# Performance work log

Measured on AMD Instinct MI355X. Metric: run time of the kernel, lower is better.

Reference implementation:

```python
import jax, jax.numpy as jnp
import numpy as np

NEG_INF = -1e30


def setup_inputs() -> dict:
    key = jax.random.key(0)
    ks = jax.random.split(key, 7)
    N, C, B = 262144, 256, 8
    feats = jax.random.normal(ks[0], (N, C), dtype=jnp.float32)
    scores = jax.random.normal(ks[1], (N, 1), dtype=jnp.float32)
    w_reg = jax.random.normal(ks[2], (C, 6), dtype=jnp.float32) * 0.01
    w_cls = jax.random.normal(ks[3], (C, 18), dtype=jnp.float32) * 0.01
    b_cls = jax.random.normal(ks[4], (18,), dtype=jnp.float32) * 0.01
    scale = jnp.ones((1,), dtype=jnp.float32)
    batch_ids = jnp.sort(jax.random.randint(ks[5], (N,), 0, B, dtype=jnp.int32))
    return {"feats": feats, "scores": scores, "w_reg": w_reg, "w_cls": w_cls,
            "b_cls": b_cls, "scale": scale, "batch_ids": batch_ids,
            "n_batches": B, "pts_threshold": 8192}


def _prune_mask(scores, batch_ids, n_batches, k):
    # scores: [N,1]; per-batch top-k selection mask (torch.topk + scatter in original).
    s = jax.lax.stop_gradient(scores[:, 0])  # computed under no_grad in torch
    # [B, N]: score where point belongs to batch b, else -inf
    per_batch = jnp.where(batch_ids[None, :] == jnp.arange(n_batches, dtype=batch_ids.dtype)[:, None],
                          s[None, :], NEG_INF)
    kth = jax.lax.top_k(per_batch, k)[0][:, -1]  # [B] k-th largest per cloud
    return s >= kth[batch_ids]  # [N] bool


def reference(feats, scores, w_reg, w_cls, b_cls, scale, batch_ids, n_batches, pts_threshold):
    mask = _prune_mask(scores, batch_ids, n_batches, pts_threshold)
    x = feats * mask[:, None].astype(feats.dtype)  # MinkowskiPruning (fixed-shape: zero out)
    # FCAF3D heads: 1x1 sparse convs == per-point matmuls; reg goes through Scale + exp.
    bbox_pred = jnp.exp(scale[0] * (x @ w_reg))          # [N, 6]
    cls_score = x @ w_cls + b_cls                         # [N, 18]
    return jnp.concatenate([bbox_pred, cls_score], axis=-1)  # [N, 24]
```

## Files before the change

kernel.cpp:

```cpp
#include <hip/hip_runtime.h>

typedef unsigned int u32;
typedef unsigned long long u64;

#define NBINS 65536
#define MAXB 8

__device__ __forceinline__ u32 mono(float f) {
    u32 u = __float_as_uint(f);
    return (u & 0x80000000u) ? ~u : (u | 0x80000000u);
}

__global__ void k_histA(const float* __restrict__ scores, const int* __restrict__ bids,
                        u32* __restrict__ hist, int N) {
    int i = blockIdx.x * blockDim.x + threadIdx.x;
    if (i >= N) return;
    atomicAdd(&hist[(u32)bids[i] * NBINS + (mono(scores[i]) >> 16)], 1u);
}

__global__ void k_histB(const float* __restrict__ scores, const int* __restrict__ bids,
                        const u32* __restrict__ Hstar, u32* __restrict__ hist, int N) {
    int i = blockIdx.x * blockDim.x + threadIdx.x;
    if (i >= N) return;
    int b = bids[i];
    u32 key = mono(scores[i]);
    if ((key >> 16) == Hstar[b])
        atomicAdd(&hist[(u32)b * NBINS + (key & 0xFFFFu)], 1u);
}

__device__ int suffix_select(const u32* __restrict__ h, u32 target, u32& remaining_out) {
    __shared__ u32 s[256];
    __shared__ int cc_s;
    __shared__ u32 run_s;
    __shared__ int res_s;
    __shared__ u32 rem_s;
    const int t = threadIdx.x;
    if (t == 0) cc_s = -1;
    u32 tot = 0;
    const uint4* hv = (const uint4*)(h + t * 256);
#pragma unroll 8
    for (int q = 0; q < 64; ++q) { uint4 v = hv[q]; tot += v.x + v.y + v.z + v.w; }
    s[t] = tot;
    __syncthreads();
    for (int off = 1; off < 256; off <<= 1) {
        u32 add = (t + off < 256) ? s[t + off] : 0u;
        __syncthreads();
        s[t] += add;
        __syncthreads();
    }
    u32 nxt = (t == 255) ? 0u : s[t + 1];
    if (s[t] >= target && nxt < target) { cc_s = t; run_s = nxt; }
    __syncthreads();
    int cc = cc_s;
    if (cc < 0) { remaining_out = 0; return -1; }
    u32 running = run_s;
    u32 v = h[cc * 256 + t];
    __syncthreads();
    s[t] = v;
    __syncthreads();
    for (int off = 1; off < 256; off <<= 1) {
        u32 add = (t + off < 256) ? s[t + off] : 0u;
        __syncthreads();
        s[t] += add;
        __syncthreads();
    }
    u32 nxt2 = (t == 255) ? 0u : s[t + 1];
    if (running + s[t] >= target && running + nxt2 < target) {
        res_s = cc * 256 + t;
        rem_s = target - (running + nxt2);
    }
    __syncthreads();
    remaining_out = rem_s;
    return res_s;
}

__global__ void k_scanA(const u32* __restrict__ hist, const int* __restrict__ kptr,
                        u32* __restrict__ Hstar, u32* __restrict__ rB,
                        u32* __restrict__ thresh) {
    int b = blockIdx.x;
    u32 rem;
    int bin = suffix_select(hist + (size_t)b * NBINS, (u32)kptr[0], rem);
    if (threadIdx.x == 0) {
        if (bin < 0) { Hstar[b] = 0xFFFFFFFFu; rB[b] = 0u; thresh[b] = 0u; }
        else { Hstar[b] = (u32)bin; rB[b] = rem; }
    }
}

__global__ void k_scanB(const u32* __restrict__ hist, const u32* __restrict__ Hstar,
                        const u32* __restrict__ rB, u32* __restrict__ thresh) {
    int b = blockIdx.x;
    u32 H = Hstar[b];
    if (H == 0xFFFFFFFFu) return;
    u32 rem;
    int bin = suffix_select(hist + (size_t)b * NBINS, rB[b], rem);
    if (threadIdx.x == 0) thresh[b] = (H << 16) | (u32)bin;
}

__global__ __launch_bounds__(256) void k_fused(
    const float* __restrict__ feats, const float* __restrict__ scores,
    const int* __restrict__ bids, const u32* __restrict__ thresh,
    const float* __restrict__ wreg, const float* __restrict__ wcls,
    const float* __restrict__ bcls, const float* __restrict__ scalep,
    float* __restrict__ out, int N) {

    __shared__ float W[256 * 24];
    __shared__ u32 alive_idx[512];
    __shared__ u32 nAlive;
    __shared__ float defrow[24];

    float scl = scalep[0];
    for (int idx = threadIdx.x; idx < 256 * 24; idx += 256) {
        int c = idx / 24, j = idx - c * 24;
        W[idx] = (j < 6) ? scl * wreg[c * 6 + j] : wcls[c * 18 + (j - 6)];
    }
    if (threadIdx.x == 0) nAlive = 0;
    if (threadIdx.x < 24) defrow[threadIdx.x] = (threadIdx.x < 6) ? 1.0f : bcls[threadIdx.x - 6];
    __syncthreads();

    const int base = blockIdx.x * 512;
#pragma unroll
    for (int q = 0; q < 2; ++q) {
        int i = base + threadIdx.x + q * 256;
        if (i < N) {
            bool alive = mono(scores[i]) >= thresh[bids[i]];
            if (alive) {
                u32 p = atomicAdd(&nAlive, 1u);
                alive_idx[p] = (u32)i;
            } else {
                float4* op = (float4*)(out + (size_t)i * 24);
                const float4* s4 = (const float4*)defrow;
#pragma unroll
                for (int w = 0; w < 6; ++w) op[w] = s4[w];
            }
        }
    }
    __syncthreads();
    const u32 cnt = nAlive;

    for (u32 r = threadIdx.x; r < cnt; r += 256) {
        u32 i = alive_idx[r];
        const float* row = feats + (size_t)i * 256;
        float acc[24];
#pragma unroll
        for (int j = 0; j < 24; ++j) acc[j] = 0.f;
        for (int c0 = 0; c0 < 256; c0 += 8) {
            float4 a = *(const float4*)(row + c0);
            float4 b = *(const float4*)(row + c0 + 4);
            float f[8] = {a.x, a.y, a.z, a.w, b.x, b.y, b.z, b.w};
#pragma unroll
            for (int t = 0; t < 8; ++t) {
                const float* wr = &W[(c0 + t) * 24];
#pragma unroll
                for (int j = 0; j < 24; j += 4) {
                    float4 w4 = *(const float4*)(wr + j);
                    acc[j + 0] += f[t] * w4.x;
                    acc[j + 1] += f[t] * w4.y;
                    acc[j + 2] += f[t] * w4.z;
                    acc[j + 3] += f[t] * w4.w;
                }
            }
        }
        __align__(16) float o[24];
#pragma unroll
        for (int j = 0; j < 6; ++j) o[j] = __expf(acc[j]);
#pragma unroll
        for (int j = 0; j < 18; ++j) o[6 + j] = acc[6 + j] + defrow[6 + j];
        float4* op = (float4*)(out + (size_t)i * 24);
        const float4* s4 = (const float4*)o;
#pragma unroll
        for (int w = 0; w < 6; ++w) op[w] = s4[w];
    }
}

extern "C" void kernel_launch(void* const* d_in, const int* in_sizes, int n_in,
                              void* d_out, int out_size, void* d_ws, size_t ws_size,
                              hipStream_t stream) {
    const float* feats  = (const float*)d_in[0];
    const float* scores = (const float*)d_in[1];
    const float* wreg   = (const float*)d_in[2];
    const float* wcls   = (const float*)d_in[3];
    const float* bcls   = (const float*)d_in[4];
    const float* scalep = (const float*)d_in[5];
    const int*   bids   = (const int*)d_in[6];
    const int*   kptr   = (const int*)d_in[8];
    float* out = (float*)d_out;
    const int N = in_sizes[6];

    u32* histA  = (u32*)d_ws;
    u32* histB  = histA + (size_t)MAXB * NBINS;
    u32* thresh = histB + (size_t)MAXB * NBINS;
    u32* Hstar  = thresh + 16;
    u32* rB     = Hstar + 16;

    hipMemsetAsync(d_ws, 0, (2 * (size_t)MAXB * NBINS) * sizeof(u32), stream);

    int nb = (N + 255) / 256;
    k_histA<<<nb, 256, 0, stream>>>(scores, bids, histA, N);
    k_scanA<<<MAXB, 256, 0, stream>>>(histA, kptr, Hstar, rB, thresh);
    k_histB<<<nb, 256, 0, stream>>>(scores, bids, Hstar, histB, N);
    k_scanB<<<MAXB, 256, 0, stream>>>(histB, Hstar, rB, thresh);
    k_fused<<<(N + 511) / 512, 256, 0, stream>>>(feats, scores, bids, thresh,
                                                 wreg, wcls, bcls, scalep, out, N);
}
```

Measured before the change: 414.2 us.

## Replace global two-pass radix select with single per-batch shared-memory select kernel

Replaces the memset, two global-atomic histogram kernels and two scan kernels with one kernel that runs one 1024-thread block per batch. Each block binary-searches its segment of the sorted batch ids and does a three-level 11/11/10-bit radix select on scores using shared-memory histograms. The fused matmul kernel also splits each alive row across two threads, each covering half the channels, and combines them with a lane shuffle. This removes the large histogram memset and launch overhead but runs the whole select on only 8 blocks, which could leave that stage serialized.

New measurement: 414.0 us. About the same (-0.1%).

```diff
diff --git a/kernel.cpp b/kernel.cpp
--- a/kernel.cpp
+++ b/kernel.cpp
@@ -3,7 +3,6 @@
 typedef unsigned int u32;
 typedef unsigned long long u64;
 
-#define NBINS 65536
 #define MAXB 8
 
 __device__ __forceinline__ u32 mono(float f) {
@@ -11,89 +10,118 @@
     return (u & 0x80000000u) ? ~u : (u | 0x80000000u);
 }
 
-__global__ void k_histA(const float* __restrict__ scores, const int* __restrict__ bids,
-                        u32* __restrict__ hist, int N) {
-    int i = blockIdx.x * blockDim.x + threadIdx.x;
-    if (i >= N) return;
-    atomicAdd(&hist[(u32)bids[i] * NBINS + (mono(scores[i]) >> 16)], 1u);
-}
-
-__global__ void k_histB(const float* __restrict__ scores, const int* __restrict__ bids,
-                        const u32* __restrict__ Hstar, u32* __restrict__ hist, int N) {
-    int i = blockIdx.x * blockDim.x + threadIdx.x;
-    if (i >= N) return;
-    int b = bids[i];
-    u32 key = mono(scores[i]);
-    if ((key >> 16) == Hstar[b])
-        atomicAdd(&hist[(u32)b * NBINS + (key & 0xFFFFu)], 1u);
-}
-
-__device__ int suffix_select(const u32* __restrict__ h, u32 target, u32& remaining_out) {
-    __shared__ u32 s[256];
-    __shared__ int cc_s;
-    __shared__ u32 run_s;
-    __shared__ int res_s;
-    __shared__ u32 rem_s;
+
+struct SelShared {
+    u32 h[2048];
+    u32 wtot[16];
+    u32 wsuf[17];
+    u32 selbin;
+    u32 selrem;
+    int deficient;
+    int cnt_s;
+};
+
+__device__ void suffix_select(SelShared* sh, int NB, u32 target) {
     const int t = threadIdx.x;
-    if (t == 0) cc_s = -1;
-    u32 tot = 0;
-    const uint4* hv = (const uint4*)(h + t * 256);
-#pragma unroll 8
-    for (int q = 0; q < 64; ++q) { uint4 v = hv[q]; tot += v.x + v.y + v.z + v.w; }
-    s[t] = tot;
-    __syncthreads();
-    for (int off = 1; off < 256; off <<= 1) {
-        u32 add = (t + off < 256) ? s[t + off] : 0u;
-        __syncthreads();
-        s[t] += add;
-        __syncthreads();
-    }
-    u32 nxt = (t == 255) ? 0u : s[t + 1];
-    if (s[t] >= target && nxt < target) { cc_s = t; run_s = nxt; }
-    __syncthreads();
-    int cc = cc_s;
-    if (cc < 0) { remaining_out = 0; return -1; }
-    u32 running = run_s;
-    u32 v = h[cc * 256 + t];
-    __syncthreads();
-    s[t] = v;
-    __syncthreads();
-    for (int off = 1; off < 256; off <<= 1) {
-        u32 add = (t + off < 256) ? s[t + off] : 0u;
-        __syncthreads();
-        s[t] += add;
-        __syncthreads();
-    }
-    u32 nxt2 = (t == 255) ? 0u : s[t + 1];
-    if (running + s[t] >= target && running + nxt2 < target) {
-        res_s = cc * 256 + t;
-        rem_s = target - (running + nxt2);
-    }
-    __syncthreads();
-    remaining_out = rem_s;
-    return res_s;
-}
-
-__global__ void k_scanA(const u32* __restrict__ hist, const int* __restrict__ kptr,
-                        u32* __restrict__ Hstar, u32* __restrict__ rB,
-                        u32* __restrict__ thresh) {
-    int b = blockIdx.x;
-    u32 rem;
-    int bin = suffix_select(hist + (size_t)b * NBINS, (u32)kptr[0], rem);
-    if (threadIdx.x == 0) {
-        if (bin < 0) { Hstar[b] = 0xFFFFFFFFu; rB[b] = 0u; thresh[b] = 0u; }
-        else { Hstar[b] = (u32)bin; rB[b] = rem; }
-    }
-}
-
-__global__ void k_scanB(const u32* __restrict__ hist, const u32* __restrict__ Hstar,
-                        const u32* __restrict__ rB, u32* __restrict__ thresh) {
-    int b = blockIdx.x;
-    u32 H = Hstar[b];
-    if (H == 0xFFFFFFFFu) return;
-    u32 rem;
-    int bin = suffix_select(hist + (size_t)b * NBINS, rB[b], rem);
-    if (threadIdx.x == 0) thresh[b] = (H << 16) | (u32)bin;
+    const int lane = t & 63;
+    const int w = t >> 6;
+    const int bpt = NB >> 10;
+    const u32 b0 = (u32)t * (u32)bpt;
+    u32 tot = sh->h[b0];
+    if (bpt == 2) tot += sh->h[b0 + 1];
+    u32 x = tot;
+#pragma unroll
+    for (int d = 1; d < 64; d <<= 1) {
+        u32 y = __shfl_down(x, d);
+        if (lane + d < 64) x += y;
+    }
+    if (lane == 0) sh->wtot[w] = x;
+    __syncthreads();
+    if (t == 0) {
+        u32 run = 0;
+        for (int i = 15; i >= 0; --i) { sh->wsuf[i] = run + sh->wtot[i]; run += sh->wtot[i]; }
+        sh->wsuf[16] = 0;
+        sh->deficient = (sh->wsuf[0] < target) ? 1 : 0;
+    }
+    __syncthreads();
+    if (sh->deficient) return;
+    u32 s_t = x + sh->wsuf[w + 1];
+    u32 s_next = s_t - tot;
+    if (s_t >= target && s_next < target) {
+        u32 run = s_next;
+        for (int q = bpt - 1; q >= 0; --q) {
+            u32 c = sh->h[b0 + q];
+            if (run + c >= target) { sh->selbin = b0 + (u32)q; sh->selrem = target - run; break; }
+            run += c;
+        }
+    }
+    __syncthreads();
+}
+
+__device__ int lb_sorted(const int* __restrict__ bids, int N, int v, SelShared* sh) {
+    const int t = threadIdx.x;
+    if (t == 0) sh->cnt_s = -1;
+    __syncthreads();
+    int nS = (N + 1023) >> 10;
+    if (t < nS && bids[t << 10] < v) atomicMax(&sh->cnt_s, t);
+    __syncthreads();
+    int c = sh->cnt_s;
+    int base = (c < 0) ? 0 : (c << 10);
+    __syncthreads();
+    if (t == 0) sh->cnt_s = 0;
+    __syncthreads();
+    int i = base + t;
+    int pred = (i < N && bids[i] < v) ? 1 : 0;
+    u64 m = __ballot(pred);
+    if ((t & 63) == 0) atomicAdd(&sh->cnt_s, (int)__popcll(m));
+    __syncthreads();
+    int cnt = sh->cnt_s;
+    __syncthreads();
+    return base + cnt;
+}
+
+__global__ __launch_bounds__(1024) void k_select(
+    const float* __restrict__ scores, const int* __restrict__ bids,
+    const int* __restrict__ kptr, u32* __restrict__ thresh, int N) {
+    __shared__ SelShared sh;
+    const int t = threadIdx.x;
+    const int b = blockIdx.x;
+    const u32 target = (u32)kptr[0];
+
+    int start = lb_sorted(bids, N, b, &sh);
+    int end   = lb_sorted(bids, N, b + 1, &sh);
+
+    for (int q = t; q < 2048; q += 1024) sh.h[q] = 0;
+    __syncthreads();
+    for (int i = start + t; i < end; i += 1024)
+        atomicAdd(&sh.h[mono(scores[i]) >> 21], 1u);
+    __syncthreads();
+    suffix_select(&sh, 2048, target);
+    if (sh.deficient) { if (t == 0) thresh[b] = 0u; return; }
+    u32 p1 = sh.selbin, r1 = sh.selrem;
+    __syncthreads();
+
+    for (int q = t; q < 2048; q += 1024) sh.h[q] = 0;
+    __syncthreads();
+    for (int i = start + t; i < end; i += 1024) {
+        u32 key = mono(scores[i]);
+        if ((key >> 21) == p1) atomicAdd(&sh.h[(key >> 10) & 0x7FFu], 1u);
+    }
+    __syncthreads();
+    suffix_select(&sh, 2048, r1);
+    u32 p2 = sh.selbin, r2 = sh.selrem;
+    __syncthreads();
+
+    for (int q = t; q < 1024; q += 1024) sh.h[q] = 0;
+    __syncthreads();
+    const u32 pref = (p1 << 11) | p2;
+    for (int i = start + t; i < end; i += 1024) {
+        u32 key = mono(scores[i]);
+        if ((key >> 10) == pref) atomicAdd(&sh.h[key & 0x3FFu], 1u);
+    }
+    __syncthreads();
+    suffix_select(&sh, 1024, r2);
+    if (t == 0) thresh[b] = (pref << 10) | sh.selbin;
 }
 
 __global__ __launch_bounds__(256) void k_fused(
@@ -137,38 +165,48 @@
     __syncthreads();
     const u32 cnt = nAlive;
 
-    for (u32 r = threadIdx.x; r < cnt; r += 256) {
+    const int h   = threadIdx.x & 1;
+    const int pid = threadIdx.x >> 1;
+    for (u32 r = pid; r < cnt; r += 128) {
         u32 i = alive_idx[r];
-        const float* row = feats + (size_t)i * 256;
+        const float* row = feats + (size_t)i * 256 + h * 128;
+        const float* Wh  = &W[h * 128 * 24];
         float acc[24];
 #pragma unroll
         for (int j = 0; j < 24; ++j) acc[j] = 0.f;
-        for (int c0 = 0; c0 < 256; c0 += 8) {
+        for (int c0 = 0; c0 < 128; c0 += 8) {
             float4 a = *(const float4*)(row + c0);
-            float4 b = *(const float4*)(row + c0 + 4);
-            float f[8] = {a.x, a.y, a.z, a.w, b.x, b.y, b.z, b.w};
-#pragma unroll
-            for (int t = 0; t < 8; ++t) {
-                const float* wr = &W[(c0 + t) * 24];
+            float4 bq = *(const float4*)(row + c0 + 4);
+            float f[8] = {a.x, a.y, a.z, a.w, bq.x, bq.y, bq.z, bq.w};
+#pragma unroll
+            for (int tt = 0; tt < 8; ++tt) {
+                const float* wr = &Wh[(c0 + tt) * 24];
 #pragma unroll
                 for (int j = 0; j < 24; j += 4) {
                     float4 w4 = *(const float4*)(wr + j);
-                    acc[j + 0] += f[t] * w4.x;
-                    acc[j + 1] += f[t] * w4.y;
-                    acc[j + 2] += f[t] * w4.z;
-                    acc[j + 3] += f[t] * w4.w;
+                    acc[j + 0] += f[tt] * w4.x;
+                    acc[j + 1] += f[tt] * w4.y;
+                    acc[j + 2] += f[tt] * w4.z;
+                    acc[j + 3] += f[tt] * w4.w;
                 }
             }
         }
-        __align__(16) float o[24];
-#pragma unroll
-        for (int j = 0; j < 6; ++j) o[j] = __expf(acc[j]);
-#pragma unroll
-        for (int j = 0; j < 18; ++j) o[6 + j] = acc[6 + j] + defrow[6 + j];
-        float4* op = (float4*)(out + (size_t)i * 24);
+#pragma unroll
+        for (int j = 0; j < 24; ++j) acc[j] += __shfl_xor(acc[j], 1);
+        __align__(16) float o[12];
+        if (h == 0) {
+#pragma unroll
+            for (int j = 0; j < 6; ++j) o[j] = __expf(acc[j]);
+#pragma unroll
+            for (int j = 6; j < 12; ++j) o[j] = acc[j] + defrow[j];
+        } else {
+#pragma unroll
+            for (int j = 0; j < 12; ++j) o[j] = acc[12 + j] + defrow[12 + j];
+        }
+        float4* op = (float4*)(out + (size_t)i * 24 + h * 12);
         const float4* s4 = (const float4*)o;
 #pragma unroll
-        for (int w = 0; w < 6; ++w) op[w] = s4[w];
+        for (int w = 0; w < 3; ++w) op[w] = s4[w];
     }
 }
 
@@ -186,19 +224,9 @@
     float* out = (float*)d_out;
     const int N = in_sizes[6];
 
-    u32* histA  = (u32*)d_ws;
-    u32* histB  = histA + (size_t)MAXB * NBINS;
-    u32* thresh = histB + (size_t)MAXB * NBINS;
-    u32* Hstar  = thresh + 16;
-    u32* rB     = Hstar + 16;
-
-    hipMemsetAsync(d_ws, 0, (2 * (size_t)MAXB * NBINS) * sizeof(u32), stream);
-
-    int nb = (N + 255) / 256;
-    k_histA<<<nb, 256, 0, stream>>>(scores, bids, histA, N);
-    k_scanA<<<MAXB, 256, 0, stream>>>(histA, kptr, Hstar, rB, thresh);
-    k_histB<<<nb, 256, 0, stream>>>(scores, bids, Hstar, histB, N);
-    k_scanB<<<MAXB, 256, 0, stream>>>(histB, Hstar, rB, thresh);
+    u32* thresh = (u32*)d_ws;
+
+    k_select<<<MAXB, 1024, 0, stream>>>(scores, bids, kptr, thresh, N);
     k_fused<<<(N + 511) / 512, 256, 0, stream>>>(feats, scores, bids, thresh,
                                                  wreg, wcls, bcls, scalep, out, N);
 }
```
